# Optimization experiments

Measured on AMD Instinct MI355X. Metric: run time of the kernel, lower is better.

Reference implementation:

```python
import jax, jax.numpy as jnp
import numpy as np


def _lstm_cell(x_t, h, c, w_ih, w_hh, b):
    # x_t, h, c: [B, 1]; w_ih, w_hh: [4, 1]; b: [4]
    # PyTorch gate order: input, forget, cell(g), output
    gates = x_t @ w_ih.T + h @ w_hh.T + b  # [B, 4]
    i, f, g, o = jnp.split(gates, 4, axis=-1)
    i = jax.nn.sigmoid(i)
    f = jax.nn.sigmoid(f)
    o = jax.nn.sigmoid(o)
    g = jnp.tanh(g)
    c = f * c + i * g
    h = o * jnp.tanh(c)
    return h, c


def setup_inputs() -> dict:
    key = jax.random.key(0)
    ks = jax.random.split(key, 8)
    B, T_IN, STEPS = 32768, 1024, 512
    return {
        "x": jax.random.normal(ks[0], (B, 1, T_IN), dtype=jnp.float32),
        "t": jax.random.normal(ks[1], (B, 1, STEPS), dtype=jnp.float32),
        "h0": jax.random.normal(ks[2], (B, 1), dtype=jnp.float32),
        "c0": jax.random.normal(ks[3], (B, 1), dtype=jnp.float32),
        "w_ih": jax.random.normal(ks[4], (4, 1), dtype=jnp.float32),
        "w_hh": jax.random.normal(ks[5], (4, 1), dtype=jnp.float32),
        "b_ih": jax.random.normal(ks[6], (4,), dtype=jnp.float32) * 0.1,
        "b_hh": jax.random.normal(ks[7], (4,), dtype=jnp.float32) * 0.1,
    }


def reference(x, t, h0, c0, w_ih, w_hh, b_ih, b_hh):
    b = b_ih + b_hh
    # open loop: feed every input timestep through the LSTM cell
    xs = jnp.transpose(x[:, 0, :], (1, 0))[:, :, None]  # [T_in, B, 1]

    def open_step(carry, x_t):
        h, c = carry
        h, c = _lstm_cell(x_t, h, c, w_ih, w_hh, b)
        return (h, c), None

    (h, c), _ = jax.lax.scan(open_step, (h0, c0), xs)

    ts = jnp.transpose(t[:, 0, :], (1, 0))[:, :, None]  # [steps, B, 1]

    def closed_step(carry, _):
        h, c, x_in = carry
        h, c = _lstm_cell(x_in, h, c, w_ih, w_hh, b)
        return (h, c, h), h

    steps = ts.shape[0]
    _, preds = jax.lax.scan(closed_step, (h, c, xs[-1]), None, length=steps)
    # criterion = MSELoss(mean), accumulated per step:
    # sum_t mean_B((pred_t - t_t)^2)
    loss = jnp.sum(jnp.mean((preds - ts) ** 2, axis=(1, 2)))
    # pred_seq is detached numpy in the original -> stop_gradient here
    pred_seq = jax.lax.stop_gradient(jnp.transpose(preds[:, :, 0], (1, 0)))  # [B, steps]
    return loss, pred_seq
```

## Files before the change

kernel.cpp:

```cpp
#include <hip/hip_runtime.h>


#define L2E 1.44269504088896340736f
#define B_TOT 32768
#define T_IN 1024
#define STEPS 512
#define CPB 32
#define CH 64
#define PAD 65

__device__ __forceinline__ float ex2(float x){ return __builtin_amdgcn_exp2f(x); }
__device__ __forceinline__ float rcp(float x){ return __builtin_amdgcn_rcpf(x); }
template<int CTRL>
__device__ __forceinline__ float qp(float v){
    return __int_as_float(__builtin_amdgcn_mov_dpp(__float_as_int(v), CTRL, 0xF, 0xF, true));
}

struct LaneK { float A1,B1,C1, A2,B2,C2, W1,W2; };

__device__ __forceinline__ void tail(float z1, float z2, float& h, float& C){
    float r1 = rcp(1.0f + ex2(z1));
    float r2 = rcp(1.0f + ex2(z2));
    float ri = qp<0xA0>(r1);
    float rf = qp<0xF5>(r1);
    float rg = qp<0xA0>(r2);
    float ro = qp<0xF5>(r2);
    float g2 = fmaf(rg, -4.0f * L2E, 2.0f * L2E);
    C = fmaf(rf, C, ri * g2);
    float e   = ex2(C);
    float ro2 = ro + ro;
    float rc  = rcp(1.0f + e);
    h = fmaf(-rc, ro2, ro);
}

__device__ __forceinline__ void stage_issue32(const float* __restrict__ base,
                                              int rs, int col0, int lane, float4* v){
    const int r_lo = lane >> 4, c4 = lane & 15;
    #pragma unroll
    for (int j = 0; j < 8; ++j)
        v[j] = *(const float4*)(base + (size_t)(j*4 + r_lo) * rs + col0 + c4*4);
}
__device__ __forceinline__ void stage_write32(float* __restrict__ lds, int lane,
                                              const float4* v){
    const int r_lo = lane >> 4, c4 = lane & 15;
    #pragma unroll
    for (int j = 0; j < 8; ++j){
        float* p = lds + (j*4 + r_lo) * PAD + c4*4;
        p[0]=v[j].x; p[1]=v[j].y; p[2]=v[j].z; p[3]=v[j].w;
    }
}

__global__ __launch_bounds__(64) void lstm_chain_kernel(
    const float* __restrict__ x, const float* __restrict__ t,
    const float* __restrict__ h0, const float* __restrict__ c0,
    const float* __restrict__ w_ih, const float* __restrict__ w_hh,
    const float* __restrict__ b_ih, const float* __restrict__ b_hh,
    float* __restrict__ out)
{
    __shared__ float sb[2][CPB * PAD];
    __shared__ float pb[CPB * PAD];

    const int lane = threadIdx.x;
    const bool odd = lane & 1;
    const int ch   = lane >> 1;
    const int b0   = blockIdx.x * CPB;

    LaneK K;
    {
        float bi = b_ih[0] + b_hh[0], bf = b_ih[1] + b_hh[1];
        float bg = b_ih[2] + b_hh[2], bo = b_ih[3] + b_hh[3];
        float Ai = -L2E*w_ih[0], Bi = -L2E*w_hh[0], Ci = -L2E*bi;
        float Af = -L2E*w_ih[1], Bf = -L2E*w_hh[1], Cf = -L2E*bf;
        float Ag = 2.0f*L2E*w_ih[2], Bg = 2.0f*L2E*w_hh[2], Cg = 2.0f*L2E*bg;
        float Ao = -L2E*w_ih[3], Bo = -L2E*w_hh[3], Co = -L2E*bo;
        K.A1 = odd ? Af : Ai;  K.B1 = odd ? Bf : Bi;  K.C1 = odd ? Cf : Ci;
        K.A2 = odd ? Ao : Ag;  K.B2 = odd ? Bo : Bg;  K.C2 = odd ? Co : Cg;
        K.W1 = K.A1 + K.B1;    K.W2 = K.A2 + K.B2;
    }

    float h = h0[b0 + ch];
    float C = (2.0f * L2E) * c0[b0 + ch];

    const float* xbase = x + (size_t)b0 * T_IN;
    const float* tbase = t + (size_t)b0 * STEPS;

    { float4 stg[8]; stage_issue32(xbase, T_IN, 0, lane, stg); stage_write32(sb[0], lane, stg); }
    #pragma unroll 1
    for (int k = 0; k < T_IN / CH; ++k){
        float4 stg[8];
        if (k < T_IN/CH - 1) stage_issue32(xbase, T_IN, (k+1)*CH, lane, stg);
        const float* xrow = &sb[k & 1][ch * PAD];
        #pragma unroll 8
        for (int s = 0; s < CH; ++s){
            float xv = xrow[s];
            float z1 = fmaf(h, K.B1, fmaf(xv, K.A1, K.C1));
            float z2 = fmaf(h, K.B2, fmaf(xv, K.A2, K.C2));
            tail(z1, z2, h, C);
        }
        if (k < T_IN/CH - 1) stage_write32(sb[(k+1) & 1], lane, stg);
    }
    float xin = sb[1][ch * PAD + (CH - 1)];

    { float4 stg[8]; stage_issue32(tbase, STEPS, 0, lane, stg); stage_write32(sb[0], lane, stg); }
    float lacc = 0.0f;
    #pragma unroll 1
    for (int k = 0; k < STEPS / CH; ++k){
        float4 stg[8];
        if (k < STEPS/CH - 1) stage_issue32(tbase, STEPS, (k+1)*CH, lane, stg);
        float* prow = &pb[ch * PAD];
        if (k == 0){
            tail(fmaf(h, K.B1, fmaf(xin, K.A1, K.C1)),
                 fmaf(h, K.B2, fmaf(xin, K.A2, K.C2)), h, C);
            prow[0] = h;
            #pragma unroll 8
            for (int s = 1; s < CH; ++s){
                tail(fmaf(h, K.W1, K.C1), fmaf(h, K.W2, K.C2), h, C);
                prow[s] = h;
            }
        } else {
            #pragma unroll 8
            for (int s = 0; s < CH; ++s){
                tail(fmaf(h, K.W1, K.C1), fmaf(h, K.W2, K.C2), h, C);
                prow[s] = h;
            }
        }
        const float* trow = &sb[k & 1][0];
        float* obase = out + 1 + (size_t)b0 * STEPS + k * CH;
        #pragma unroll 4
        for (int r = 0; r < CPB; ++r){
            float p  = pb[r * PAD + lane];
            float tv = trow[r * PAD + lane];
            float d  = p - tv;
            lacc = fmaf(d, d, lacc);
            obase[(size_t)r * STEPS + lane] = p;
        }
        if (k < STEPS/CH - 1) stage_write32(sb[(k+1) & 1], lane, stg);
    }

    #pragma unroll
    for (int off = 32; off > 0; off >>= 1)
        lacc += __shfl_down(lacc, off, 64);
    if (lane == 0)
        atomicAdd(out, lacc * (1.0f / (float)B_TOT));
}

extern "C" void kernel_launch(void* const* d_in, const int* in_sizes, int n_in,
                              void* d_out, int out_size, void* d_ws, size_t ws_size,
                              hipStream_t stream) {
    const float* x    = (const float*)d_in[0];
    const float* t    = (const float*)d_in[1];
    const float* h0   = (const float*)d_in[2];
    const float* c0   = (const float*)d_in[3];
    const float* w_ih = (const float*)d_in[4];
    const float* w_hh = (const float*)d_in[5];
    const float* b_ih = (const float*)d_in[6];
    const float* b_hh = (const float*)d_in[7];
    float* out = (float*)d_out;

    hipMemsetAsync(out, 0, sizeof(float), stream);

    lstm_chain_kernel<<<B_TOT / CPB, 64, 0, stream>>>(
        x, t, h0, c0, w_ih, w_hh, b_ih, b_hh, out);
}
```

Before: 316.4 us.

## Split each LSTM chain across four lanes, one gate per lane

Each batch chain now runs on a quad of lanes, one gate per lane, instead of a pair of lanes each computing two gates. Chains per block drop from 32 to 16, which doubles the grid, and the gate values are exchanged with quad-broadcast DPP moves. Staging loads and LDS tiles shrink to match. The aim is to cut per-step instruction latency on the serial recurrence and put more waves on each SIMD to hide it. The cost is half as many chains per wave, so twice as many waves in total, and the sigmoid/tanh tail is repeated redundantly across four lanes.

New measurement: 320.4 us. About the same (+1.3%).

```diff
diff --git a/kernel.cpp b/kernel.cpp
--- a/kernel.cpp
+++ b/kernel.cpp
@@ -5,7 +5,7 @@
 #define B_TOT 32768
 #define T_IN 1024
 #define STEPS 512
-#define CPB 32
+#define CPB 16
 #define CH 64
 #define PAD 65
 
@@ -16,35 +16,35 @@
     return __int_as_float(__builtin_amdgcn_mov_dpp(__float_as_int(v), CTRL, 0xF, 0xF, true));
 }
 
-struct LaneK { float A1,B1,C1, A2,B2,C2, W1,W2; };
+struct LaneK { float A, Bh, Cc, W; };
 
-__device__ __forceinline__ void tail(float z1, float z2, float& h, float& C){
-    float r1 = rcp(1.0f + ex2(z1));
-    float r2 = rcp(1.0f + ex2(z2));
-    float ri = qp<0xA0>(r1);
-    float rf = qp<0xF5>(r1);
-    float rg = qp<0xA0>(r2);
-    float ro = qp<0xF5>(r2);
+__device__ __forceinline__ void tail(float z, float& h, float& C){
+    float e  = ex2(z);
+    float r  = rcp(1.0f + e);
+    float ri = qp<0x00>(r);
+    float rf = qp<0x55>(r);
+    float rg = qp<0xAA>(r);
+    float ro = qp<0xFF>(r);
     float g2 = fmaf(rg, -4.0f * L2E, 2.0f * L2E);
     C = fmaf(rf, C, ri * g2);
-    float e   = ex2(C);
+    float eC  = ex2(C);
     float ro2 = ro + ro;
-    float rc  = rcp(1.0f + e);
+    float rc  = rcp(1.0f + eC);
     h = fmaf(-rc, ro2, ro);
 }
 
-__device__ __forceinline__ void stage_issue32(const float* __restrict__ base,
+__device__ __forceinline__ void stage_issue16(const float* __restrict__ base,
                                               int rs, int col0, int lane, float4* v){
     const int r_lo = lane >> 4, c4 = lane & 15;
     #pragma unroll
-    for (int j = 0; j < 8; ++j)
+    for (int j = 0; j < 4; ++j)
         v[j] = *(const float4*)(base + (size_t)(j*4 + r_lo) * rs + col0 + c4*4);
 }
-__device__ __forceinline__ void stage_write32(float* __restrict__ lds, int lane,
+__device__ __forceinline__ void stage_write16(float* __restrict__ lds, int lane,
                                               const float4* v){
     const int r_lo = lane >> 4, c4 = lane & 15;
     #pragma unroll
-    for (int j = 0; j < 8; ++j){
+    for (int j = 0; j < 4; ++j){
         float* p = lds + (j*4 + r_lo) * PAD + c4*4;
         p[0]=v[j].x; p[1]=v[j].y; p[2]=v[j].z; p[3]=v[j].w;
     }
@@ -61,21 +61,19 @@
     __shared__ float pb[CPB * PAD];
 
     const int lane = threadIdx.x;
-    const bool odd = lane & 1;
-    const int ch   = lane >> 1;
+    const int role = lane & 3;
+    const int ch   = lane >> 2;
     const int b0   = blockIdx.x * CPB;
 
     LaneK K;
     {
-        float bi = b_ih[0] + b_hh[0], bf = b_ih[1] + b_hh[1];
-        float bg = b_ih[2] + b_hh[2], bo = b_ih[3] + b_hh[3];
-        float Ai = -L2E*w_ih[0], Bi = -L2E*w_hh[0], Ci = -L2E*bi;
-        float Af = -L2E*w_ih[1], Bf = -L2E*w_hh[1], Cf = -L2E*bf;
-        float Ag = 2.0f*L2E*w_ih[2], Bg = 2.0f*L2E*w_hh[2], Cg = 2.0f*L2E*bg;
-        float Ao = -L2E*w_ih[3], Bo = -L2E*w_hh[3], Co = -L2E*bo;
-        K.A1 = odd ? Af : Ai;  K.B1 = odd ? Bf : Bi;  K.C1 = odd ? Cf : Ci;
-        K.A2 = odd ? Ao : Ag;  K.B2 = odd ? Bo : Bg;  K.C2 = odd ? Co : Cg;
-        K.W1 = K.A1 + K.B1;    K.W2 = K.A2 + K.B2;
+        float wih = w_ih[role], whh = w_hh[role];
+        float bb  = b_ih[role] + b_hh[role];
+        float sc  = (role == 2) ? (2.0f * L2E) : (-L2E);
+        K.A  = sc * wih;
+        K.Bh = sc * whh;
+        K.Cc = sc * bb;
+        K.W  = K.A + K.Bh;
     }
 
     float h = h0[b0 + ch];
@@ -84,43 +82,41 @@
     const float* xbase = x + (size_t)b0 * T_IN;
     const float* tbase = t + (size_t)b0 * STEPS;
 
-    { float4 stg[8]; stage_issue32(xbase, T_IN, 0, lane, stg); stage_write32(sb[0], lane, stg); }
+    { float4 stg[4]; stage_issue16(xbase, T_IN, 0, lane, stg); stage_write16(sb[0], lane, stg); }
     #pragma unroll 1
     for (int k = 0; k < T_IN / CH; ++k){
-        float4 stg[8];
-        if (k < T_IN/CH - 1) stage_issue32(xbase, T_IN, (k+1)*CH, lane, stg);
+        float4 stg[4];
+        if (k < T_IN/CH - 1) stage_issue16(xbase, T_IN, (k+1)*CH, lane, stg);
         const float* xrow = &sb[k & 1][ch * PAD];
         #pragma unroll 8
         for (int s = 0; s < CH; ++s){
             float xv = xrow[s];
-            float z1 = fmaf(h, K.B1, fmaf(xv, K.A1, K.C1));
-            float z2 = fmaf(h, K.B2, fmaf(xv, K.A2, K.C2));
-            tail(z1, z2, h, C);
+            float z = fmaf(h, K.Bh, fmaf(xv, K.A, K.Cc));
+            tail(z, h, C);
         }
-        if (k < T_IN/CH - 1) stage_write32(sb[(k+1) & 1], lane, stg);
+        if (k < T_IN/CH - 1) stage_write16(sb[(k+1) & 1], lane, stg);
     }
     float xin = sb[1][ch * PAD + (CH - 1)];
 
-    { float4 stg[8]; stage_issue32(tbase, STEPS, 0, lane, stg); stage_write32(sb[0], lane, stg); }
+    { float4 stg[4]; stage_issue16(tbase, STEPS, 0, lane, stg); stage_write16(sb[0], lane, stg); }
     float lacc = 0.0f;
     #pragma unroll 1
     for (int k = 0; k < STEPS / CH; ++k){
-        float4 stg[8];
-        if (k < STEPS/CH - 1) stage_issue32(tbase, STEPS, (k+1)*CH, lane, stg);
+        float4 stg[4];
+        if (k < STEPS/CH - 1) stage_issue16(tbase, STEPS, (k+1)*CH, lane, stg);
         float* prow = &pb[ch * PAD];
         if (k == 0){
-            tail(fmaf(h, K.B1, fmaf(xin, K.A1, K.C1)),
-                 fmaf(h, K.B2, fmaf(xin, K.A2, K.C2)), h, C);
+            tail(fmaf(h, K.Bh, fmaf(xin, K.A, K.Cc)), h, C);
             prow[0] = h;
             #pragma unroll 8
             for (int s = 1; s < CH; ++s){
-                tail(fmaf(h, K.W1, K.C1), fmaf(h, K.W2, K.C2), h, C);
+                tail(fmaf(h, K.W, K.Cc), h, C);
                 prow[s] = h;
             }
         } else {
             #pragma unroll 8
             for (int s = 0; s < CH; ++s){
-                tail(fmaf(h, K.W1, K.C1), fmaf(h, K.W2, K.C2), h, C);
+                tail(fmaf(h, K.W, K.Cc), h, C);
                 prow[s] = h;
             }
         }
@@ -134,7 +130,7 @@
             lacc = fmaf(d, d, lacc);
             obase[(size_t)r * STEPS + lane] = p;
         }
-        if (k < STEPS/CH - 1) stage_write32(sb[(k+1) & 1], lane, stg);
+        if (k < STEPS/CH - 1) stage_write16(sb[(k+1) & 1], lane, stg);
     }
 
     #pragma unroll
```
